# Optimization experiments

Hardware: AMD Instinct MI355X
Metric: run time of the kernel (lower is better)

The kernel has to match this reference:

```python
import jax, jax.numpy as jnp
import numpy as np

NUM_GRIDS, G, F, N, D = 8, 96, 16, 1048576, 3


def setup_inputs() -> dict:
    key = jax.random.key(0)
    k1, k2, k3 = jax.random.split(key, 3)
    voxel_embeddings = jax.random.normal(k1, (NUM_GRIDS, G, G, G, F), dtype=jnp.float32)
    grid_indexes = jax.random.randint(k2, (N, 1), 0, NUM_GRIDS, dtype=jnp.int32)
    # points in [-1, 1]^3 (module remaps to [0, 1])
    points = jax.random.uniform(k3, (N, D), dtype=jnp.float32, minval=-1.0, maxval=1.0)
    return {"voxel_embeddings": voxel_embeddings, "grid_indexes": grid_indexes, "points": points}


def _strides(shape):
    out, s = [], 1
    for x in reversed(shape):
        out.append(s)
        s *= x
    return list(reversed(out))


def reference(voxel_embeddings, grid_indexes, points):
    grid_shape = voxel_embeddings.shape[1:-1]          # (G, G, G)
    num_features = voxel_embeddings.shape[-1]
    d = points.shape[-1]
    gs = jnp.asarray(grid_shape, dtype=jnp.int32)      # [D]

    p = (points + 1.0) * 0.5                           # remap to [0,1]
    scaled = p * (gs - 1)                              # [..., D] float
    base = scaled.astype(jnp.int32)                    # truncation, as in original
    frac = scaled - base                               # fractional coords [..., D]

    # corner offsets: bit i of corner k toggles dim i (matches compute_corner_indices order)
    k = jnp.arange(2 ** d, dtype=jnp.int32)
    offsets = (k[:, None] >> jnp.arange(d, dtype=jnp.int32)[None, :]) & 1  # [2^D, D]
    corners = jnp.clip(base[..., None, :] + offsets, 0, gs - 1)            # [..., 2^D, D]

    # linearized gather over flattened [num_grids, *grid_shape]
    spatial_strides = jnp.asarray(_strides(voxel_embeddings.shape[:-1]), dtype=jnp.int32)  # [D+1]
    gi = jnp.broadcast_to(grid_indexes[..., None, :], (*corners.shape[:-1], 1))            # [..., 2^D, 1]
    full_idx = jnp.concatenate([gi, corners], axis=-1)                                      # [..., 2^D, D+1]
    lin = jnp.sum(full_idx * spatial_strides, axis=-1)                                      # [..., 2^D]
    values_flat = voxel_embeddings.reshape(-1, num_features)
    latents = values_flat[lin]                                                              # [..., 2^D, F]

    # trilinear weights: prod over dims of frac (if corner bit set) or 1-frac
    w = jnp.prod(jnp.where(offsets.astype(bool), frac[..., None, :], 1.0 - frac[..., None, :]), axis=-1)  # [..., 2^D]
    out = jnp.sum(latents * w[..., None], axis=-2)                                          # [..., F]

    inside = jnp.all((p >= 0.0) & (p <= 1.0), axis=-1, keepdims=True)
    return out * inside
```

## Files before the change

### kernel.cpp

```cpp
#include <hip/hip_runtime.h>


#define GDIM 96
#define NFEAT 16

__global__ __launch_bounds__(256) void grid_interp_kernel(
    const float* __restrict__ vox,
    const int*   __restrict__ gidx,
    const float* __restrict__ pts,
    float*       __restrict__ out,
    int n_total)
{
    const int stride = gridDim.x * blockDim.x;
    for (int tid = blockIdx.x * blockDim.x + threadIdx.x; tid < n_total; tid += stride) {
        const int p = tid >> 4;
        const int f = tid & 15;

        const float px = pts[p * 3 + 0];
        const float py = pts[p * 3 + 1];
        const float pz = pts[p * 3 + 2];
        const int   gi = gidx[p];

        const float ux = (px + 1.0f) * 0.5f;
        const float uy = (py + 1.0f) * 0.5f;
        const float uz = (pz + 1.0f) * 0.5f;
        const bool inside = (ux >= 0.0f) & (ux <= 1.0f) &
                            (uy >= 0.0f) & (uy <= 1.0f) &
                            (uz >= 0.0f) & (uz <= 1.0f);

        const float sx = ux * (float)(GDIM - 1);
        const float sy = uy * (float)(GDIM - 1);
        const float sz = uz * (float)(GDIM - 1);
        const int bx = (int)sx, by = (int)sy, bz = (int)sz;
        const float fx = sx - (float)bx;
        const float fy = sy - (float)by;
        const float fz = sz - (float)bz;

        const int gbase = gi * (GDIM * GDIM * GDIM);

        float acc = 0.0f;
#pragma unroll
        for (int k = 0; k < 8; ++k) {
            const int ox = (k >> 0) & 1;
            const int oy = (k >> 1) & 1;
            const int oz = (k >> 2) & 1;
            int cx = bx + ox; cx = cx < 0 ? 0 : (cx > GDIM - 1 ? GDIM - 1 : cx);
            int cy = by + oy; cy = cy < 0 ? 0 : (cy > GDIM - 1 ? GDIM - 1 : cy);
            int cz = bz + oz; cz = cz < 0 ? 0 : (cz > GDIM - 1 ? GDIM - 1 : cz);
            const int vidx = ((gbase + cx * (GDIM * GDIM) + cy * GDIM + cz) << 4) + f;
            const float w = (ox ? fx : 1.0f - fx) *
                            (oy ? fy : 1.0f - fy) *
                            (oz ? fz : 1.0f - fz);
            acc = fmaf(vox[vidx], w, acc);
        }

        out[tid] = inside ? acc : 0.0f;
    }
}

extern "C" void kernel_launch(void* const* d_in, const int* in_sizes, int n_in,
                              void* d_out, int out_size, void* d_ws, size_t ws_size,
                              hipStream_t stream) {
    const float* vox  = (const float*)d_in[0];
    const int*   gidx = (const int*)  d_in[1];
    const float* pts  = (const float*)d_in[2];
    float*       outp = (float*)d_out;

    const int n_pts   = in_sizes[1];
    const int n_total = n_pts * NFEAT;

    const int threads = 256;
    const int blocks  = 8192;

    grid_interp_kernel<<<blocks, threads, 0, stream>>>(vox, gidx, pts, outp, n_total);
}
```

Before: 137.9 us.

## Split interpolation into per-grid passes with wave-cooperative corner gathers

Launches one pass per grid, so each pass only touches one grid's voxel table (about 56 MB) and has a better chance of reuse in the last-level cache. Inside a pass, each wave ballots the points in its 64-point chunk that belong to the current grid and processes them one at a time. The four 16-lane groups take the four x/y corner pairs, each loading two z-neighbours, and the partial sums are combined with cross-lane shuffles. The cost is eight launches that each re-read all points and indices, and per-point serial loops where only 16 lanes write results.

Result: slower. 223.2 us (+61.8%).

```diff
diff --git a/kernel.cpp b/kernel.cpp
--- a/kernel.cpp
+++ b/kernel.cpp
@@ -3,23 +3,46 @@
 
 #define GDIM 96
 #define NFEAT 16
+#define NGRIDS 8
 
-__global__ __launch_bounds__(256) void grid_interp_kernel(
+__global__ __launch_bounds__(256) void grid_interp_pass(
     const float* __restrict__ vox,
     const int*   __restrict__ gidx,
     const float* __restrict__ pts,
     float*       __restrict__ out,
-    int n_total)
+    int n_pts, int g)
 {
-    const int stride = gridDim.x * blockDim.x;
-    for (int tid = blockIdx.x * blockDim.x + threadIdx.x; tid < n_total; tid += stride) {
-        const int p = tid >> 4;
-        const int f = tid & 15;
+    const int lane  = threadIdx.x & 63;
+    const int wavei = (blockIdx.x * (blockDim.x >> 6)) + (threadIdx.x >> 6);
+    const int pbase = wavei * 64;
+    if (pbase >= n_pts) return;
 
-        const float px = pts[p * 3 + 0];
-        const float py = pts[p * 3 + 1];
-        const float pz = pts[p * 3 + 2];
-        const int   gi = gidx[p];
+    const int p_lane = pbase + lane;
+    const bool valid = (p_lane < n_pts);
+
+    const int gv = valid ? gidx[p_lane] : -1;
+    float plx = 0.f, ply = 0.f, plz = 0.f;
+    if (valid) {
+        plx = pts[p_lane * 3 + 0];
+        ply = pts[p_lane * 3 + 1];
+        plz = pts[p_lane * 3 + 2];
+    }
+
+    unsigned long long mask = __ballot(gv == g);
+
+    const int cg = lane >> 4;
+    const int f  = lane & 15;
+    const int ox = cg & 1;
+    const int oy = (cg >> 1) & 1;
+
+    while (mask) {
+        const int poff = __builtin_ctzll(mask);
+        mask &= mask - 1;
+        const int p = pbase + poff;
+
+        const float px = __shfl(plx, poff, 64);
+        const float py = __shfl(ply, poff, 64);
+        const float pz = __shfl(plz, poff, 64);
 
         const float ux = (px + 1.0f) * 0.5f;
         const float uy = (py + 1.0f) * 0.5f;
@@ -36,25 +59,26 @@
         const float fy = sy - (float)by;
         const float fz = sz - (float)bz;
 
-        const int gbase = gi * (GDIM * GDIM * GDIM);
+        int cx = bx + ox; cx = cx < 0 ? 0 : (cx > GDIM - 1 ? GDIM - 1 : cx);
+        int cy = by + oy; cy = cy < 0 ? 0 : (cy > GDIM - 1 ? GDIM - 1 : cy);
+        int cz0 = bz;     cz0 = cz0 < 0 ? 0 : (cz0 > GDIM - 1 ? GDIM - 1 : cz0);
+        int cz1 = bz + 1; cz1 = cz1 < 0 ? 0 : (cz1 > GDIM - 1 ? GDIM - 1 : cz1);
 
-        float acc = 0.0f;
-#pragma unroll
-        for (int k = 0; k < 8; ++k) {
-            const int ox = (k >> 0) & 1;
-            const int oy = (k >> 1) & 1;
-            const int oz = (k >> 2) & 1;
-            int cx = bx + ox; cx = cx < 0 ? 0 : (cx > GDIM - 1 ? GDIM - 1 : cx);
-            int cy = by + oy; cy = cy < 0 ? 0 : (cy > GDIM - 1 ? GDIM - 1 : cy);
-            int cz = bz + oz; cz = cz < 0 ? 0 : (cz > GDIM - 1 ? GDIM - 1 : cz);
-            const int vidx = ((gbase + cx * (GDIM * GDIM) + cy * GDIM + cz) << 4) + f;
-            const float w = (ox ? fx : 1.0f - fx) *
-                            (oy ? fy : 1.0f - fy) *
-                            (oz ? fz : 1.0f - fz);
-            acc = fmaf(vox[vidx], w, acc);
+        const int cellbase = ((g * GDIM + cx) * GDIM + cy) * GDIM;
+        const float v0 = vox[(cellbase + cz0) * NFEAT + f];
+        const float v1 = vox[(cellbase + cz1) * NFEAT + f];
+
+        const float wx  = ox ? fx : 1.0f - fx;
+        const float wy  = oy ? fy : 1.0f - fy;
+        const float wxy = wx * wy;
+        float acc = wxy * fmaf(fz, v1, (1.0f - fz) * v0);
+
+        acc += __shfl_xor(acc, 16, 64);
+        acc += __shfl_xor(acc, 32, 64);
+
+        if (lane < NFEAT) {
+            out[p * NFEAT + lane] = inside ? acc : 0.0f;
         }
-
-        out[tid] = inside ? acc : 0.0f;
     }
 }
 
@@ -66,11 +90,11 @@
     const float* pts  = (const float*)d_in[2];
     float*       outp = (float*)d_out;
 
-    const int n_pts   = in_sizes[1];
-    const int n_total = n_pts * NFEAT;
+    const int n_pts = in_sizes[1];
+    const int threads = 256;
+    const int blocks  = (n_pts + 255) / 256;
 
-    const int threads = 256;
-    const int blocks  = 8192;
-
-    grid_interp_kernel<<<blocks, threads, 0, stream>>>(vox, gidx, pts, outp, n_total);
+    for (int g = 0; g < NGRIDS; ++g) {
+        grid_interp_pass<<<blocks, threads, 0, stream>>>(vox, gidx, pts, outp, n_pts, g);
+    }
 }
```

## Bucket points by spatial region before gathering voxel features

Applied to the files above, without the earlier changes.

Adds a three-kernel path: zero the bucket counters, bin points into spatial buckets (grid × coarse x/y/z block) with atomics, then gather per bucket using float4 feature loads. Points in the same region then hit nearby voxels together, which is meant to improve cache locality for the random 8-corner gathers. Buckets that overflow are computed directly in the binning kernel. The cost is extra launches, the atomics, and writing and reading point data in workspace. The path runs only if the workspace is large enough; otherwise the original dense kernel runs.

Result: slower. 372.9 us (+170.3%).

```diff
diff --git a/kernel.cpp b/kernel.cpp
--- a/kernel.cpp
+++ b/kernel.cpp
@@ -1,10 +1,139 @@
 #include <hip/hip_runtime.h>
 
 
-#define GDIM 96
-#define NFEAT 16
-
-__global__ __launch_bounds__(256) void grid_interp_kernel(
+#define GDIM   96
+#define NFEAT  16
+#define NGRIDS 8
+#define SBX 6
+#define SBY 6
+#define SBZ 3
+#define NBUCK (NGRIDS * SBX * SBY * SBZ)
+#define CAP 2048
+
+__device__ __forceinline__ int clampi(int v, int lo, int hi) {
+    return v < lo ? lo : (v > hi ? hi : v);
+}
+
+__global__ void zero_cnt_kernel(int* __restrict__ cnt) {
+    const int i = blockIdx.x * blockDim.x + threadIdx.x;
+    if (i < NBUCK) cnt[i] = 0;
+}
+
+__global__ __launch_bounds__(256) void bucket_kernel(
+    const float* __restrict__ vox,
+    const int*   __restrict__ gidx,
+    const float* __restrict__ pts,
+    float*       __restrict__ out,
+    float4*      __restrict__ slots,
+    int*         __restrict__ cnt,
+    int n_pts)
+{
+    const int p = blockIdx.x * blockDim.x + threadIdx.x;
+    if (p >= n_pts) return;
+
+    const float px = pts[3 * p + 0];
+    const float py = pts[3 * p + 1];
+    const float pz = pts[3 * p + 2];
+    int gi = gidx[p];
+    gi = clampi(gi, 0, NGRIDS - 1);
+
+    const float ux = (px + 1.0f) * 0.5f;
+    const float uy = (py + 1.0f) * 0.5f;
+    const float uz = (pz + 1.0f) * 0.5f;
+    const int bx = clampi((int)(ux * (float)(GDIM - 1)), 0, GDIM - 1);
+    const int by = clampi((int)(uy * (float)(GDIM - 1)), 0, GDIM - 1);
+    const int bz = clampi((int)(uz * (float)(GDIM - 1)), 0, GDIM - 1);
+
+    const int key = ((gi * SBX + (bx >> 4)) * SBY + (by >> 4)) * SBZ + (bz >> 5);
+    const int pos = atomicAdd(&cnt[key], 1);
+
+    if (pos < CAP) {
+        float4 s;
+        s.x = px; s.y = py; s.z = pz; s.w = __int_as_float(p);
+        slots[key * CAP + pos] = s;
+    } else {
+        const float sx = ux * (float)(GDIM - 1);
+        const float sy = uy * (float)(GDIM - 1);
+        const float sz = uz * (float)(GDIM - 1);
+        const int ibx = (int)sx, iby = (int)sy, ibz = (int)sz;
+        const float fx = sx - (float)ibx, fy = sy - (float)iby, fz = sz - (float)ibz;
+        const bool inside = (ux >= 0.f) & (ux <= 1.f) & (uy >= 0.f) & (uy <= 1.f) &
+                            (uz >= 0.f) & (uz <= 1.f);
+        for (int f = 0; f < NFEAT; ++f) {
+            float acc = 0.f;
+            for (int k = 0; k < 8; ++k) {
+                const int ox = k & 1, oy = (k >> 1) & 1, oz = (k >> 2) & 1;
+                const int cx = clampi(ibx + ox, 0, GDIM - 1);
+                const int cy = clampi(iby + oy, 0, GDIM - 1);
+                const int cz = clampi(ibz + oz, 0, GDIM - 1);
+                const float w = (ox ? fx : 1.f - fx) * (oy ? fy : 1.f - fy) * (oz ? fz : 1.f - fz);
+                acc = fmaf(vox[(((gi * GDIM + cx) * GDIM + cy) * GDIM + cz) * NFEAT + f], w, acc);
+            }
+            out[p * NFEAT + f] = inside ? acc : 0.f;
+        }
+    }
+}
+
+__global__ __launch_bounds__(256) void gather_kernel(
+    const float*  __restrict__ vox,
+    const float4* __restrict__ slots,
+    const int*    __restrict__ cnt,
+    float*        __restrict__ out)
+{
+    const int bucket = blockIdx.x >> 2;
+    const int q      = blockIdx.x & 3;
+    int cb = cnt[bucket];
+    cb = cb > CAP ? CAP : cb;
+    const int lo = (cb * q) >> 2;
+    const int hi = (cb * (q + 1)) >> 2;
+
+    const int gi = bucket / (SBX * SBY * SBZ);
+    const int f4 = (threadIdx.x & 3) << 2;
+    const float4* __restrict__ base = slots + (size_t)bucket * CAP;
+
+    for (int s = lo + (int)(threadIdx.x >> 2); s < hi; s += 64) {
+        const float4 sd = base[s];
+        const int p = __float_as_int(sd.w);
+
+        const float ux = (sd.x + 1.0f) * 0.5f;
+        const float uy = (sd.y + 1.0f) * 0.5f;
+        const float uz = (sd.z + 1.0f) * 0.5f;
+        const bool inside = (ux >= 0.f) & (ux <= 1.f) & (uy >= 0.f) & (uy <= 1.f) &
+                            (uz >= 0.f) & (uz <= 1.f);
+
+        const float sx = ux * (float)(GDIM - 1);
+        const float sy = uy * (float)(GDIM - 1);
+        const float sz = uz * (float)(GDIM - 1);
+        const int bx = (int)sx, by = (int)sy, bz = (int)sz;
+        const float fx = sx - (float)bx;
+        const float fy = sy - (float)by;
+        const float fz = sz - (float)bz;
+
+        float ax = 0.f, ay = 0.f, az = 0.f, aw = 0.f;
+#pragma unroll
+        for (int k = 0; k < 8; ++k) {
+            const int ox = k & 1, oy = (k >> 1) & 1, oz = (k >> 2) & 1;
+            const int cx = clampi(bx + ox, 0, GDIM - 1);
+            const int cy = clampi(by + oy, 0, GDIM - 1);
+            const int cz = clampi(bz + oz, 0, GDIM - 1);
+            const float4 v = *(const float4*)&vox[(size_t)((((gi * GDIM + cx) * GDIM + cy) * GDIM + cz) * NFEAT + f4)];
+            const float w = (ox ? fx : 1.f - fx) * (oy ? fy : 1.f - fy) * (oz ? fz : 1.f - fz);
+            ax = fmaf(v.x, w, ax);
+            ay = fmaf(v.y, w, ay);
+            az = fmaf(v.z, w, az);
+            aw = fmaf(v.w, w, aw);
+        }
+
+        float4 r;
+        r.x = inside ? ax : 0.f;
+        r.y = inside ? ay : 0.f;
+        r.z = inside ? az : 0.f;
+        r.w = inside ? aw : 0.f;
+        *(float4*)&out[(size_t)p * NFEAT + f4] = r;
+    }
+}
+
+__global__ __launch_bounds__(256) void grid_interp_dense(
     const float* __restrict__ vox,
     const int*   __restrict__ gidx,
     const float* __restrict__ pts,
@@ -15,45 +144,31 @@
     for (int tid = blockIdx.x * blockDim.x + threadIdx.x; tid < n_total; tid += stride) {
         const int p = tid >> 4;
         const int f = tid & 15;
-
         const float px = pts[p * 3 + 0];
         const float py = pts[p * 3 + 1];
         const float pz = pts[p * 3 + 2];
-        const int   gi = gidx[p];
-
+        const int gi = gidx[p];
         const float ux = (px + 1.0f) * 0.5f;
         const float uy = (py + 1.0f) * 0.5f;
         const float uz = (pz + 1.0f) * 0.5f;
-        const bool inside = (ux >= 0.0f) & (ux <= 1.0f) &
-                            (uy >= 0.0f) & (uy <= 1.0f) &
-                            (uz >= 0.0f) & (uz <= 1.0f);
-
+        const bool inside = (ux >= 0.f) & (ux <= 1.f) & (uy >= 0.f) & (uy <= 1.f) &
+                            (uz >= 0.f) & (uz <= 1.f);
         const float sx = ux * (float)(GDIM - 1);
         const float sy = uy * (float)(GDIM - 1);
         const float sz = uz * (float)(GDIM - 1);
         const int bx = (int)sx, by = (int)sy, bz = (int)sz;
-        const float fx = sx - (float)bx;
-        const float fy = sy - (float)by;
-        const float fz = sz - (float)bz;
-
+        const float fx = sx - (float)bx, fy = sy - (float)by, fz = sz - (float)bz;
         const int gbase = gi * (GDIM * GDIM * GDIM);
-
         float acc = 0.0f;
 #pragma unroll
         for (int k = 0; k < 8; ++k) {
-            const int ox = (k >> 0) & 1;
-            const int oy = (k >> 1) & 1;
-            const int oz = (k >> 2) & 1;
-            int cx = bx + ox; cx = cx < 0 ? 0 : (cx > GDIM - 1 ? GDIM - 1 : cx);
-            int cy = by + oy; cy = cy < 0 ? 0 : (cy > GDIM - 1 ? GDIM - 1 : cy);
-            int cz = bz + oz; cz = cz < 0 ? 0 : (cz > GDIM - 1 ? GDIM - 1 : cz);
-            const int vidx = ((gbase + cx * (GDIM * GDIM) + cy * GDIM + cz) << 4) + f;
-            const float w = (ox ? fx : 1.0f - fx) *
-                            (oy ? fy : 1.0f - fy) *
-                            (oz ? fz : 1.0f - fz);
-            acc = fmaf(vox[vidx], w, acc);
+            const int ox = k & 1, oy = (k >> 1) & 1, oz = (k >> 2) & 1;
+            const int cx = clampi(bx + ox, 0, GDIM - 1);
+            const int cy = clampi(by + oy, 0, GDIM - 1);
+            const int cz = clampi(bz + oz, 0, GDIM - 1);
+            const float w = (ox ? fx : 1.f - fx) * (oy ? fy : 1.f - fy) * (oz ? fz : 1.f - fz);
+            acc = fmaf(vox[((gbase + cx * GDIM * GDIM + cy * GDIM + cz) << 4) + f], w, acc);
         }
-
         out[tid] = inside ? acc : 0.0f;
     }
 }
@@ -66,11 +181,20 @@
     const float* pts  = (const float*)d_in[2];
     float*       outp = (float*)d_out;
 
-    const int n_pts   = in_sizes[1];
-    const int n_total = n_pts * NFEAT;
-
-    const int threads = 256;
-    const int blocks  = 8192;
-
-    grid_interp_kernel<<<blocks, threads, 0, stream>>>(vox, gidx, pts, outp, n_total);
-}
+    const int n_pts = in_sizes[1];
+
+    const size_t slots_off = 4096;
+    const size_t needed = slots_off + (size_t)NBUCK * CAP * sizeof(float4);
+
+    if (ws_size < needed) {
+        grid_interp_dense<<<8192, 256, 0, stream>>>(vox, gidx, pts, outp, n_pts * NFEAT);
+        return;
+    }
+
+    int*    cnt   = (int*)d_ws;
+    float4* slots = (float4*)((char*)d_ws + slots_off);
+
+    zero_cnt_kernel<<<(NBUCK + 255) / 256, 256, 0, stream>>>(cnt);
+    bucket_kernel<<<(n_pts + 255) / 256, 256, 0, stream>>>(vox, gidx, pts, outp, slots, cnt, n_pts);
+    gather_kernel<<<NBUCK * 4, 256, 0, stream>>>(vox, slots, cnt, outp);
+}
```

## Vectorize feature gather to float4 per thread and use nontemporal point I/O

Applied to the files above, without the earlier changes.

Each thread now handles four features of a point with 16-byte vector loads from the voxel grid and a vector store to the output, instead of one scalar feature per thread. This cuts the number of load instructions and the repeated per-point coordinate and weight math by four. Point and index loads and the output store are marked nontemporal so they bypass cache retention. The grid-stride loop becomes a one-task-per-thread launch sized to the work, which raises the block count.

Result: faster. 133.3 us (median of 2 runs) (-3.4%).

```diff
diff --git a/kernel.cpp b/kernel.cpp
--- a/kernel.cpp
+++ b/kernel.cpp
@@ -1,76 +1,89 @@
 #include <hip/hip_runtime.h>
 
 
-#define GDIM 96
+#define GDIM  96
 #define NFEAT 16
 
-__global__ __launch_bounds__(256) void grid_interp_kernel(
-    const float* __restrict__ vox,
+typedef float f32x4 __attribute__((ext_vector_type(4)));
+
+__device__ __forceinline__ int clampi(int v, int lo, int hi) {
+    return v < lo ? lo : (v > hi ? hi : v);
+}
+
+__global__ __launch_bounds__(256) void grid_interp_v4(
+    const f32x4* __restrict__ vox4,
     const int*   __restrict__ gidx,
     const float* __restrict__ pts,
-    float*       __restrict__ out,
-    int n_total)
+    f32x4*       __restrict__ out4,
+    int n_tasks)
 {
-    const int stride = gridDim.x * blockDim.x;
-    for (int tid = blockIdx.x * blockDim.x + threadIdx.x; tid < n_total; tid += stride) {
-        const int p = tid >> 4;
-        const int f = tid & 15;
+    const int tid = blockIdx.x * blockDim.x + threadIdx.x;
+    if (tid >= n_tasks) return;
 
-        const float px = pts[p * 3 + 0];
-        const float py = pts[p * 3 + 1];
-        const float pz = pts[p * 3 + 2];
-        const int   gi = gidx[p];
+    const int p  = tid >> 2;
+    const int fq = tid & 3;
 
-        const float ux = (px + 1.0f) * 0.5f;
-        const float uy = (py + 1.0f) * 0.5f;
-        const float uz = (pz + 1.0f) * 0.5f;
-        const bool inside = (ux >= 0.0f) & (ux <= 1.0f) &
-                            (uy >= 0.0f) & (uy <= 1.0f) &
-                            (uz >= 0.0f) & (uz <= 1.0f);
+    const float px = __builtin_nontemporal_load(&pts[p * 3 + 0]);
+    const float py = __builtin_nontemporal_load(&pts[p * 3 + 1]);
+    const float pz = __builtin_nontemporal_load(&pts[p * 3 + 2]);
+    const int   gi = __builtin_nontemporal_load(&gidx[p]);
 
-        const float sx = ux * (float)(GDIM - 1);
-        const float sy = uy * (float)(GDIM - 1);
-        const float sz = uz * (float)(GDIM - 1);
-        const int bx = (int)sx, by = (int)sy, bz = (int)sz;
-        const float fx = sx - (float)bx;
-        const float fy = sy - (float)by;
-        const float fz = sz - (float)bz;
+    const float ux = (px + 1.0f) * 0.5f;
+    const float uy = (py + 1.0f) * 0.5f;
+    const float uz = (pz + 1.0f) * 0.5f;
+    const bool inside = (ux >= 0.0f) & (ux <= 1.0f) &
+                        (uy >= 0.0f) & (uy <= 1.0f) &
+                        (uz >= 0.0f) & (uz <= 1.0f);
 
-        const int gbase = gi * (GDIM * GDIM * GDIM);
+    const float sx = ux * (float)(GDIM - 1);
+    const float sy = uy * (float)(GDIM - 1);
+    const float sz = uz * (float)(GDIM - 1);
+    const int bx = (int)sx, by = (int)sy, bz = (int)sz;
+    const float fx = sx - (float)bx;
+    const float fy = sy - (float)by;
+    const float fz = sz - (float)bz;
 
-        float acc = 0.0f;
+    const int gbase = gi * (GDIM * GDIM * GDIM);
+
+    float ax = 0.f, ay = 0.f, az = 0.f, aw = 0.f;
 #pragma unroll
-        for (int k = 0; k < 8; ++k) {
-            const int ox = (k >> 0) & 1;
-            const int oy = (k >> 1) & 1;
-            const int oz = (k >> 2) & 1;
-            int cx = bx + ox; cx = cx < 0 ? 0 : (cx > GDIM - 1 ? GDIM - 1 : cx);
-            int cy = by + oy; cy = cy < 0 ? 0 : (cy > GDIM - 1 ? GDIM - 1 : cy);
-            int cz = bz + oz; cz = cz < 0 ? 0 : (cz > GDIM - 1 ? GDIM - 1 : cz);
-            const int vidx = ((gbase + cx * (GDIM * GDIM) + cy * GDIM + cz) << 4) + f;
-            const float w = (ox ? fx : 1.0f - fx) *
-                            (oy ? fy : 1.0f - fy) *
-                            (oz ? fz : 1.0f - fz);
-            acc = fmaf(vox[vidx], w, acc);
-        }
+    for (int k = 0; k < 8; ++k) {
+        const int ox = k & 1, oy = (k >> 1) & 1, oz = (k >> 2) & 1;
+        const int cx = clampi(bx + ox, 0, GDIM - 1);
+        const int cy = clampi(by + oy, 0, GDIM - 1);
+        const int cz = clampi(bz + oz, 0, GDIM - 1);
+        const int cell = gbase + cx * (GDIM * GDIM) + cy * GDIM + cz;
+        const f32x4 v = vox4[(size_t)(cell << 2) + fq];
+        const float w = (ox ? fx : 1.0f - fx) *
+                        (oy ? fy : 1.0f - fy) *
+                        (oz ? fz : 1.0f - fz);
+        ax = fmaf(v.x, w, ax);
+        ay = fmaf(v.y, w, ay);
+        az = fmaf(v.z, w, az);
+        aw = fmaf(v.w, w, aw);
+    }
 
-        out[tid] = inside ? acc : 0.0f;
-    }
+    f32x4 r;
+    r.x = inside ? ax : 0.f;
+    r.y = inside ? ay : 0.f;
+    r.z = inside ? az : 0.f;
+    r.w = inside ? aw : 0.f;
+    __builtin_nontemporal_store(r, &out4[tid]);
 }
 
 extern "C" void kernel_launch(void* const* d_in, const int* in_sizes, int n_in,
                               void* d_out, int out_size, void* d_ws, size_t ws_size,
                               hipStream_t stream) {
-    const float* vox  = (const float*)d_in[0];
+    const f32x4* vox4 = (const f32x4*)d_in[0];
     const int*   gidx = (const int*)  d_in[1];
     const float* pts  = (const float*)d_in[2];
-    float*       outp = (float*)d_out;
+    f32x4*       out4 = (f32x4*)d_out;
 
     const int n_pts   = in_sizes[1];
-    const int n_total = n_pts * NFEAT;
+    const int n_tasks = n_pts * 4;
 
     const int threads = 256;
-    const int blocks  = 8192;
+    const int blocks  = (n_tasks + threads - 1) / threads;
 
-    grid_interp_kernel<<<blocks, threads, 0, stream>>>(vox, gidx, pts, outp, n_total);
+    grid_interp_v4<<<blocks, threads, 0, stream>>>(vox4, gidx, pts, out4, n_tasks);
 }
```
